# Performance work log

Measured on AMD Instinct MI355X. Metric: run time of the kernel, lower is better.

## Reference

```python
import jax, jax.numpy as jnp
import numpy as np

N_NODES = 100000


def _gcn_norm(edge_index, edge_weight, num_nodes):
    # PyG gcn_norm: add self-loops (weight 1), symmetric D^-1/2 (A+I) D^-1/2
    row, col = edge_index[0], edge_index[1]
    loop = jnp.arange(num_nodes, dtype=edge_index.dtype)
    row = jnp.concatenate([row, loop])
    col = jnp.concatenate([col, loop])
    w = jnp.concatenate([edge_weight, jnp.ones((num_nodes,), edge_weight.dtype)])
    deg = jax.ops.segment_sum(w, col, num_segments=num_nodes)
    dis = jnp.where(deg > 0, jax.lax.rsqrt(jnp.maximum(deg, 1e-12)), 0.0)
    norm = dis[row] * w * dis[col]
    return row, col, norm


def _gcn_conv(x, W, b, row, col, norm):
    h = x @ W                                   # transform first (small out dim)
    msg = norm[:, None] * h[row]                # gather + scale  [E+N, out]
    out = jax.ops.segment_sum(msg, col, num_segments=x.shape[0])  # scatter-add
    return out + b


def setup_inputs() -> dict:
    key = jax.random.key(0)
    k = jax.random.split(key, 6)
    N, E, F_IN, H, C = N_NODES, 3200000, 512, 16, 40
    x = jax.random.normal(k[0], (N, F_IN), dtype=jnp.float32)
    edge_index = jax.random.randint(k[1], (2, E), 0, N, dtype=jnp.int32)
    edge_weight = jax.random.uniform(k[2], (E,), dtype=jnp.float32)
    W1 = jax.random.normal(k[3], (F_IN, H), dtype=jnp.float32) * (1.0 / np.sqrt(F_IN))
    b1 = jnp.zeros((H,), jnp.float32)
    W2 = jax.random.normal(k[4], (H, C), dtype=jnp.float32) * (1.0 / np.sqrt(H))
    b2 = jnp.zeros((C,), jnp.float32)
    return {"x": x, "edge_index": edge_index, "edge_weight": edge_weight,
            "W1": W1, "b1": b1, "W2": W2, "b2": b2}


def reference(x, edge_index, edge_weight, W1, b1, W2, b2):
    row, col, norm = _gcn_norm(edge_index, edge_weight, N_NODES)
    h = jax.nn.relu(_gcn_conv(x, W1, b1, row, col, norm))
    # dropout is identity in eval mode
    h = _gcn_conv(h, W2, b2, row, col, norm)
    return jax.nn.log_softmax(h, axis=1)
```

## Files before the change

kernel.cpp:

```cpp
#include <hip/hip_runtime.h>
#include <math.h>

#define F_IN 512
#define HID  16
#define NCLS 40
#define NPB  128
#define NPW  2048
#define MAXBUK 1024
#define CAP  5120
#define SCAP 4608

typedef __attribute__((ext_vector_type(8))) short short8;
typedef __attribute__((ext_vector_type(4))) float floatx4;

__device__ __forceinline__ unsigned short bf16_rne(float f) {
    unsigned u = __float_as_uint(f);
    u += 0x7fffu + ((u >> 16) & 1u);
    return (unsigned short)(u >> 16);
}
__device__ __forceinline__ float bf16_f32(unsigned short s) {
    return __uint_as_float(((unsigned)s) << 16);
}

__global__ void k_zero(int* __restrict__ gcur, int nbuk) {
    int i = blockIdx.x * 256 + threadIdx.x;
    if (i < nbuk) gcur[i] = i * CAP;
}

__global__ void k_part(const int* __restrict__ row, const int* __restrict__ col,
                       const float* __restrict__ wt, int* __restrict__ gcur,
                       uint2* __restrict__ sedge, int E, int chunk, int nbuk) {
    __shared__ int lcnt[MAXBUK];
    __shared__ int lcur[MAXBUK];
    int t = threadIdx.x;
    int s = blockIdx.x * chunk;
    int e = s + chunk; if (e > E) e = E;
    if (e <= s) return;
    for (int i = t; i < nbuk; i += 256) lcnt[i] = 0;
    __syncthreads();
    for (int j = s + t; j < e; j += 256)
        atomicAdd(&lcnt[col[j] >> 7], 1);
    __syncthreads();
    for (int b = t; b < nbuk; b += 256) {
        int c = lcnt[b];
        lcur[b] = c ? atomicAdd(&gcur[b], c) : 0;
    }
    __syncthreads();
    for (int j = s + t; j < e; j += 256) {
        int r = row[j], cc = col[j];
        int b = cc >> 7;
        int slot = atomicAdd(&lcur[b], 1);
        if (slot < (b + 1) * CAP)
            sedge[slot] = make_uint2((unsigned)r | ((unsigned)(cc & (NPB - 1)) << 17),
                                     __float_as_uint(wt[j]));
    }
}

__global__ void k_sort(const uint2* __restrict__ sedge, const int* __restrict__ gcur,
                       uint2* __restrict__ sedge2, int2* __restrict__ rowse,
                       float* __restrict__ dis, int N, int nbuk) {
    __shared__ uint2 ebuf[SCAP];
    __shared__ int   cnt[NPB];
    __shared__ float wdeg[NPB];
    __shared__ int   scn[NPB];
    __shared__ int   cur[NPB];
    int b = blockIdx.x, t = threadIdx.x;
    if (t < NPB) { cnt[t] = 0; wdeg[t] = 1.0f; }
    __syncthreads();
    int s = b * CAP;
    int e = gcur[b];
    int n = e - s;
    bool fit = (n <= SCAP);
    for (int j = s + t; j < e; j += 256) {
        uint2 rec = sedge[j];
        if (fit) ebuf[j - s] = rec;
        int lc = rec.x >> 17;
        atomicAdd(&cnt[lc], 1);
        atomicAdd(&wdeg[lc], __uint_as_float(rec.y));
    }
    __syncthreads();
    if (t < NPB) scn[t] = cnt[t];
    __syncthreads();
    for (int off = 1; off < NPB; off <<= 1) {
        int a = (t < NPB && t >= off) ? scn[t - off] : 0;
        __syncthreads();
        if (t < NPB) scn[t] += a;
        __syncthreads();
    }
    if (t < NPB) {
        int excl = scn[t] - cnt[t];
        cur[t] = s + excl;
        int nn = b * NPB + t;
        if (nn < N) {
            rowse[nn] = make_int2(s + excl, s + excl + cnt[t]);
            dis[nn] = rsqrtf(wdeg[t]);
        }
    }
    __syncthreads();
    for (int i = t; i < n; i += 256) {
        uint2 rec = fit ? ebuf[i] : sedge[s + i];
        int lc = rec.x >> 17;
        int pos = atomicAdd(&cur[lc], 1);
        sedge2[pos] = make_uint2(rec.x & 0x1FFFF, rec.y);
    }
}

__global__ void k_xw1_mfma(const float* __restrict__ x, const float* __restrict__ W1,
                           const float* __restrict__ dis, float* __restrict__ h1,
                           int N, int nTiles) {
    __shared__ unsigned short wh[HID][F_IN + 8];
    __shared__ unsigned short wl[HID][F_IN + 8];
    for (int f = threadIdx.x; f < F_IN * HID; f += 256) {
        int k = f >> 4, h = f & 15;
        float v = W1[f];
        unsigned short hhi = bf16_rne(v);
        float rem = v - bf16_f32(hhi);
        wh[h][k] = hhi;
        wl[h][k] = (unsigned short)(__float_as_uint(rem) >> 16);
    }
    __syncthreads();

    int wave = threadIdx.x >> 6;
    int lane = threadIdx.x & 63;
    int tile = blockIdx.x * 4 + wave;
    if (tile >= nTiles) return;

    int m    = lane & 15;
    int quad = lane >> 4;
    int node = tile * 16 + m;
    if (node >= N) node = N - 1;
    const float* xr = x + (size_t)node * F_IN;

    floatx4 acc = {0.f, 0.f, 0.f, 0.f};

    #pragma unroll 4
    for (int s = 0; s < F_IN / 32; ++s) {
        int k0 = s * 32 + quad * 8;
        float4 v0 = *(const float4*)(xr + k0);
        float4 v1 = *(const float4*)(xr + k0 + 4);
        float xv[8] = {v0.x, v0.y, v0.z, v0.w, v1.x, v1.y, v1.z, v1.w};
        short8 ah, al;
        #pragma unroll
        for (int j = 0; j < 8; ++j) {
            unsigned u = __float_as_uint(xv[j]);
            ah[j] = (short)(u >> 16);
            float rem = xv[j] - __uint_as_float(u & 0xffff0000u);
            al[j] = (short)(__float_as_uint(rem) >> 16);
        }
        short8 bh = *(const short8*)&wh[m][k0];
        short8 bl = *(const short8*)&wl[m][k0];
        acc = __builtin_amdgcn_mfma_f32_16x16x32_bf16(ah, bh, acc, 0, 0, 0);
        acc = __builtin_amdgcn_mfma_f32_16x16x32_bf16(ah, bl, acc, 0, 0, 0);
        acc = __builtin_amdgcn_mfma_f32_16x16x32_bf16(al, bh, acc, 0, 0, 0);
    }

    int h = lane & 15;
    #pragma unroll
    for (int r = 0; r < 4; ++r) {
        int nrow = tile * 16 + quad * 4 + r;
        if (nrow < N) h1[(size_t)nrow * HID + h] = dis[nrow] * acc[r];
    }
}

__global__ void k_agg2(const uint2* __restrict__ sedge2, const int2* __restrict__ rowse,
                       const float* __restrict__ dis, const float* __restrict__ src,
                       const float* __restrict__ bias, float* __restrict__ dst,
                       int N, int relu, int postscale) {
    int g = (blockIdx.x * 256 + threadIdx.x) >> 4;
    int h = threadIdx.x & 15;
    if (g >= N) return;
    int2 se = rowse[g];
    int e1 = se.y;
    float acc = 0.f;
    int j = se.x;
    for (; j + 4 <= e1; j += 4) {
        uint2 r0 = sedge2[j + 0];
        uint2 r1 = sedge2[j + 1];
        uint2 r2 = sedge2[j + 2];
        uint2 r3 = sedge2[j + 3];
        float v0 = src[(size_t)r0.x * HID + h];
        float v1 = src[(size_t)r1.x * HID + h];
        float v2 = src[(size_t)r2.x * HID + h];
        float v3 = src[(size_t)r3.x * HID + h];
        acc = fmaf(__uint_as_float(r0.y), v0, acc);
        acc = fmaf(__uint_as_float(r1.y), v1, acc);
        acc = fmaf(__uint_as_float(r2.y), v2, acc);
        acc = fmaf(__uint_as_float(r3.y), v3, acc);
    }
    for (; j < e1; ++j) {
        uint2 r = sedge2[j];
        acc = fmaf(__uint_as_float(r.y), src[(size_t)r.x * HID + h], acc);
    }
    float d = dis[g];
    float v = d * (acc + src[(size_t)g * HID + h]);
    if (bias) v += bias[h];
    if (relu) v = v > 0.f ? v : 0.f;
    if (postscale) v *= d;
    dst[(size_t)g * HID + h] = v;
}

__global__ void k_final(const float* __restrict__ B, const float* __restrict__ W2,
                        const float* __restrict__ b2, float* __restrict__ out, int N) {
    __shared__ float w2s[HID * NCLS];
    __shared__ float b2s[NCLS];
    for (int f = threadIdx.x; f < HID * NCLS; f += 256) w2s[f] = W2[f];
    if (threadIdx.x < NCLS) b2s[threadIdx.x] = b2[threadIdx.x];
    __syncthreads();
    int nd = blockIdx.x * 256 + threadIdx.x;
    if (nd < N) {
        float a[HID];
        const float4* ap = (const float4*)(B + (size_t)nd * HID);
        #pragma unroll
        for (int q = 0; q < 4; ++q) {
            float4 v = ap[q];
            a[q * 4 + 0] = v.x; a[q * 4 + 1] = v.y;
            a[q * 4 + 2] = v.z; a[q * 4 + 3] = v.w;
        }
        float y[NCLS];
        #pragma unroll
        for (int c = 0; c < NCLS; ++c) y[c] = b2s[c];
        #pragma unroll
        for (int hh = 0; hh < HID; ++hh) {
            float av = a[hh];
            #pragma unroll
            for (int c = 0; c < NCLS; ++c) y[c] = fmaf(av, w2s[hh * NCLS + c], y[c]);
        }
        float m = y[0];
        #pragma unroll
        for (int c = 1; c < NCLS; ++c) m = fmaxf(m, y[c]);
        float sum = 0.f;
        #pragma unroll
        for (int c = 0; c < NCLS; ++c) sum += expf(y[c] - m);
        float bse = m + logf(sum);
        float* op = out + (size_t)nd * NCLS;
        #pragma unroll
        for (int c = 0; c < NCLS; ++c) op[c] = y[c] - bse;
    }
}

extern "C" void kernel_launch(void* const* d_in, const int* in_sizes, int n_in,
                              void* d_out, int out_size, void* d_ws, size_t ws_size,
                              hipStream_t stream) {
    const float* x  = (const float*)d_in[0];
    const int*   ei = (const int*)d_in[1];
    const float* ew = (const float*)d_in[2];
    const float* W1 = (const float*)d_in[3];
    const float* b1 = (const float*)d_in[4];
    const float* W2 = (const float*)d_in[5];
    const float* b2 = (const float*)d_in[6];
    float* out = (float*)d_out;

    int N = in_sizes[0] / F_IN;
    int E = in_sizes[2];
    const int* row = ei;
    const int* col = ei + E;

    int nbuk  = (N + NPB - 1) / NPB;
    int chunk = (E + NPW - 1) / NPW;

    char* w = (char*)d_ws;
    uint2* sedge  = (uint2*)w;                     size_t off = (size_t)nbuk * CAP * 8;
    uint2* sedge2 = (uint2*)(w + off);             off += (size_t)nbuk * CAP * 8;
    float* A      = (float*)(w + off);             off += (size_t)N * HID * 4;
    float* Bb     = (float*)(w + off);             off += (size_t)N * HID * 4;
    float* dis    = (float*)(w + off);             off += (size_t)N * 4;
    int2*  rowse  = (int2*)(w + off);              off += (size_t)N * 8;
    int*   gcur   = (int*)(w + off);               off += (size_t)nbuk * 4;

    dim3 blk(256);

    k_zero<<<dim3((nbuk + 255) / 256), blk, 0, stream>>>(gcur, nbuk);
    k_part<<<dim3(NPW), blk, 0, stream>>>(row, col, ew, gcur, sedge, E, chunk, nbuk);

    k_sort<<<dim3(nbuk), blk, 0, stream>>>(sedge, gcur, sedge2, rowse, dis, N, nbuk);

    int nTiles = (N + 15) / 16;
    int gT = (nTiles + 3) / 4;
    k_xw1_mfma<<<dim3(gT), blk, 0, stream>>>(x, W1, dis, A, N, nTiles);

    int gA = (N * HID + 255) / 256;
    k_agg2<<<dim3(gA), blk, 0, stream>>>(sedge2, rowse, dis, A, b1, Bb, N, 1, 1);
    k_agg2<<<dim3(gA), blk, 0, stream>>>(sedge2, rowse, dis, Bb, (const float*)nullptr, A, N, 0, 0);

    k_final<<<dim3((N + 255) / 256), blk, 0, stream>>>(A, W2, b2, out, N);
}
```

Measured before the change: 580.5 us.

## Replace single-pass bucket partition with two-level slice/bucket radix split

Result: faster. 527.7 us (-9.1%).

```diff
diff --git a/kernel.cpp b/kernel.cpp
--- a/kernel.cpp
+++ b/kernel.cpp
@@ -5,10 +5,13 @@
 #define HID  16
 #define NCLS 40
 #define NPB  128
+#define NSL  8
+#define BPS  98
+#define SLCAP 405504
+#define CAP  4608
 #define NPW  2048
-#define MAXBUK 1024
-#define CAP  5120
-#define SCAP 4608
+#define CPW2 256
+#define CH1  1600
 
 typedef __attribute__((ext_vector_type(8))) short short8;
 typedef __attribute__((ext_vector_type(4))) float floatx4;
@@ -22,58 +25,153 @@
     return __uint_as_float(((unsigned)s) << 16);
 }
 
-__global__ void k_zero(int* __restrict__ gcur, int nbuk) {
+__global__ void k_zero(int* __restrict__ gcur, int* __restrict__ scur, int nbuk) {
     int i = blockIdx.x * 256 + threadIdx.x;
     if (i < nbuk) gcur[i] = i * CAP;
-}
-
-__global__ void k_part(const int* __restrict__ row, const int* __restrict__ col,
-                       const float* __restrict__ wt, int* __restrict__ gcur,
-                       uint2* __restrict__ sedge, int E, int chunk, int nbuk) {
-    __shared__ int lcnt[MAXBUK];
-    __shared__ int lcur[MAXBUK];
+    if (i < NSL) scur[i] = i * SLCAP;
+}
+
+__global__ void k_split(const int* __restrict__ row, const int* __restrict__ col,
+                        const float* __restrict__ wt, int* __restrict__ scur,
+                        uint2* __restrict__ gstr, int E, int chunk) {
+    __shared__ uint2 recs[CH1];
+    __shared__ unsigned char bks[CH1];
+    __shared__ int cnt8[NSL], cur8[NSL], delta8[NSL];
     int t = threadIdx.x;
-    int s = blockIdx.x * chunk;
-    int e = s + chunk; if (e > E) e = E;
-    if (e <= s) return;
-    for (int i = t; i < nbuk; i += 256) lcnt[i] = 0;
-    __syncthreads();
-    for (int j = s + t; j < e; j += 256)
-        atomicAdd(&lcnt[col[j] >> 7], 1);
-    __syncthreads();
-    for (int b = t; b < nbuk; b += 256) {
-        int c = lcnt[b];
-        lcur[b] = c ? atomicAdd(&gcur[b], c) : 0;
-    }
-    __syncthreads();
-    for (int j = s + t; j < e; j += 256) {
-        int r = row[j], cc = col[j];
-        int b = cc >> 7;
-        int slot = atomicAdd(&lcur[b], 1);
-        if (slot < (b + 1) * CAP)
-            sedge[slot] = make_uint2((unsigned)r | ((unsigned)(cc & (NPB - 1)) << 17),
-                                     __float_as_uint(wt[j]));
+    int s0 = blockIdx.x * chunk;
+    int e0 = s0 + chunk; if (e0 > E) e0 = E;
+    int n = e0 - s0;
+    if (n <= 0) return;
+
+    if (n <= CH1) {
+        if (t < NSL) cnt8[t] = 0;
+        __syncthreads();
+        for (int j = s0 + t; j < e0; j += 256)
+            atomicAdd(&cnt8[(col[j] >> 7) / BPS], 1);
+        __syncthreads();
+        if (t == 0) {
+            int run = 0;
+            for (int i = 0; i < NSL; ++i) { cur8[i] = run; run += cnt8[i]; }
+        }
+        __syncthreads();
+        if (t < NSL) {
+            int c = cnt8[t];
+            int start = cur8[t];
+            int res = c ? atomicAdd(&scur[t], c) : 0;
+            delta8[t] = res - start;
+        }
+        __syncthreads();
+        for (int j = s0 + t; j < e0; j += 256) {
+            int r = row[j], cc = col[j];
+            int b = cc >> 7;
+            int sl = b / BPS;
+            int bsl = b - sl * BPS;
+            int slot = atomicAdd(&cur8[sl], 1);
+            recs[slot] = make_uint2((unsigned)r | ((unsigned)(cc & (NPB - 1)) << 17) |
+                                    ((unsigned)bsl << 24),
+                                    __float_as_uint(wt[j]));
+            bks[slot] = (unsigned char)sl;
+        }
+        __syncthreads();
+        for (int i = t; i < n; i += 256) {
+            int sl = bks[i];
+            int dst = delta8[sl] + i;
+            if ((unsigned)(dst - sl * SLCAP) < SLCAP) gstr[dst] = recs[i];
+        }
+    } else {
+        for (int j = s0 + t; j < e0; j += 256) {
+            int r = row[j], cc = col[j];
+            int b = cc >> 7;
+            int sl = b / BPS;
+            int bsl = b - sl * BPS;
+            int pos = atomicAdd(&scur[sl], 1);
+            if ((unsigned)(pos - sl * SLCAP) < SLCAP)
+                gstr[pos] = make_uint2((unsigned)r | ((unsigned)(cc & (NPB - 1)) << 17) |
+                                       ((unsigned)bsl << 24),
+                                       __float_as_uint(wt[j]));
+        }
+    }
+}
+
+__global__ void k_part2(const uint2* __restrict__ gstr, const int* __restrict__ scur,
+                        int* __restrict__ gcur, uint2* __restrict__ sedge, int nbuk) {
+    __shared__ uint2 recs[CH1];
+    __shared__ unsigned char bks[CH1];
+    __shared__ int lcnt[BPS], lcur[BPS], ldelta[BPS];
+    __shared__ int scn[128];
+    int t = threadIdx.x;
+    int sl = blockIdx.x & 7;
+    int ci = blockIdx.x >> 3;
+    int sbeg = sl * SLCAP;
+    int send = scur[sl];
+    int ns = send - sbeg;
+    int ch = (ns + CPW2 - 1) / CPW2;
+    int s0 = sbeg + ci * ch;
+    int e0 = s0 + ch; if (e0 > send) e0 = send;
+    int n = e0 - s0;
+    if (n <= 0) return;
+    for (int i = t; i < BPS; i += 256) lcnt[i] = 0;
+    __syncthreads();
+    for (int j = s0 + t; j < e0; j += 256)
+        atomicAdd(&lcnt[gstr[j].x >> 24], 1);
+    __syncthreads();
+    if (t < 128) scn[t] = (t < BPS) ? lcnt[t] : 0;
+    __syncthreads();
+    for (int off = 1; off < 128; off <<= 1) {
+        int a = (t < 128 && t >= off) ? scn[t - off] : 0;
+        __syncthreads();
+        if (t < 128) scn[t] += a;
+        __syncthreads();
+    }
+    if (t < BPS) {
+        int c = lcnt[t];
+        int start = scn[t] - c;
+        lcur[t] = start;
+        int res = c ? atomicAdd(&gcur[sl * BPS + t], c) : 0;
+        ldelta[t] = res - start;
+    }
+    __syncthreads();
+    for (int j = s0 + t; j < e0; j += 256) {
+        uint2 rec = gstr[j];
+        int bsl = rec.x >> 24;
+        int slot = atomicAdd(&lcur[bsl], 1);
+        recs[slot] = rec;
+        bks[slot] = (unsigned char)bsl;
+    }
+    __syncthreads();
+    for (int i = t; i < n; i += 256) {
+        int bsl = bks[i];
+        int gb = sl * BPS + bsl;
+        int dst = ldelta[bsl] + i;
+        if (dst < (gb + 1) * CAP) {
+            uint2 rr = recs[i];
+            rr.x &= 0x00FFFFFFu;
+            sedge[dst] = rr;
+        }
     }
 }
 
 __global__ void k_sort(const uint2* __restrict__ sedge, const int* __restrict__ gcur,
                        uint2* __restrict__ sedge2, int2* __restrict__ rowse,
                        float* __restrict__ dis, int N, int nbuk) {
-    __shared__ uint2 ebuf[SCAP];
+    __shared__ uint2 ebuf[CAP];
     __shared__ int   cnt[NPB];
     __shared__ float wdeg[NPB];
     __shared__ int   scn[NPB];
     __shared__ int   cur[NPB];
-    int b = blockIdx.x, t = threadIdx.x;
+    int sl = blockIdx.x & 7;
+    int bi = blockIdx.x >> 3;
+    int b = sl * BPS + bi;
+    if (bi >= BPS || b >= nbuk) return;
+    int t = threadIdx.x;
     if (t < NPB) { cnt[t] = 0; wdeg[t] = 1.0f; }
     __syncthreads();
     int s = b * CAP;
     int e = gcur[b];
     int n = e - s;
-    bool fit = (n <= SCAP);
     for (int j = s + t; j < e; j += 256) {
         uint2 rec = sedge[j];
-        if (fit) ebuf[j - s] = rec;
+        ebuf[j - s] = rec;
         int lc = rec.x >> 17;
         atomicAdd(&cnt[lc], 1);
         atomicAdd(&wdeg[lc], __uint_as_float(rec.y));
@@ -98,7 +196,7 @@
     }
     __syncthreads();
     for (int i = t; i < n; i += 256) {
-        uint2 rec = fit ? ebuf[i] : sedge[s + i];
+        uint2 rec = ebuf[i];
         int lc = rec.x >> 17;
         int pos = atomicAdd(&cur[lc], 1);
         sedge2[pos] = make_uint2(rec.x & 0x1FFFF, rec.y);
@@ -165,10 +263,14 @@
 __global__ void k_agg2(const uint2* __restrict__ sedge2, const int2* __restrict__ rowse,
                        const float* __restrict__ dis, const float* __restrict__ src,
                        const float* __restrict__ bias, float* __restrict__ dst,
-                       int N, int relu, int postscale) {
-    int g = (blockIdx.x * 256 + threadIdx.x) >> 4;
+                       int N, int nbuk, int relu, int postscale) {
+    int sl  = blockIdx.x & 7;
+    int loc = blockIdx.x >> 3;
+    int b   = sl * BPS + (loc >> 3);
+    int sub = loc & 7;
+    int g = b * NPB + sub * 16 + (threadIdx.x >> 4);
     int h = threadIdx.x & 15;
-    if (g >= N) return;
+    if (b >= nbuk || g >= N) return;
     int2 se = rowse[g];
     int e1 = se.y;
     float acc = 0.f;
@@ -259,28 +361,30 @@
     int chunk = (E + NPW - 1) / NPW;
 
     char* w = (char*)d_ws;
-    uint2* sedge  = (uint2*)w;                     size_t off = (size_t)nbuk * CAP * 8;
+    uint2* gstr   = (uint2*)w;                     size_t off = (size_t)NSL * SLCAP * 8;
+    uint2* sedge  = (uint2*)(w + off);             off += (size_t)nbuk * CAP * 8;
     uint2* sedge2 = (uint2*)(w + off);             off += (size_t)nbuk * CAP * 8;
     float* A      = (float*)(w + off);             off += (size_t)N * HID * 4;
     float* Bb     = (float*)(w + off);             off += (size_t)N * HID * 4;
     float* dis    = (float*)(w + off);             off += (size_t)N * 4;
     int2*  rowse  = (int2*)(w + off);              off += (size_t)N * 8;
     int*   gcur   = (int*)(w + off);               off += (size_t)nbuk * 4;
+    int*   scur   = (int*)(w + off);               off += (size_t)NSL * 4;
 
     dim3 blk(256);
 
-    k_zero<<<dim3((nbuk + 255) / 256), blk, 0, stream>>>(gcur, nbuk);
-    k_part<<<dim3(NPW), blk, 0, stream>>>(row, col, ew, gcur, sedge, E, chunk, nbuk);
-
-    k_sort<<<dim3(nbuk), blk, 0, stream>>>(sedge, gcur, sedge2, rowse, dis, N, nbuk);
+    k_zero<<<dim3((nbuk + 255) / 256), blk, 0, stream>>>(gcur, scur, nbuk);
+    k_split<<<dim3(NPW), blk, 0, stream>>>(row, col, ew, scur, gstr, E, chunk);
+    k_part2<<<dim3(NSL * CPW2), blk, 0, stream>>>(gstr, scur, gcur, sedge, nbuk);
+
+    k_sort<<<dim3(NSL * BPS), blk, 0, stream>>>(sedge, gcur, sedge2, rowse, dis, N, nbuk);
 
     int nTiles = (N + 15) / 16;
     int gT = (nTiles + 3) / 4;
     k_xw1_mfma<<<dim3(gT), blk, 0, stream>>>(x, W1, dis, A, N, nTiles);
 
-    int gA = (N * HID + 255) / 256;
-    k_agg2<<<dim3(gA), blk, 0, stream>>>(sedge2, rowse, dis, A, b1, Bb, N, 1, 1);
-    k_agg2<<<dim3(gA), blk, 0, stream>>>(sedge2, rowse, dis, Bb, (const float*)nullptr, A, N, 0, 0);
+    k_agg2<<<dim3(NSL * BPS * 8), blk, 0, stream>>>(sedge2, rowse, dis, A, b1, Bb, N, nbuk, 1, 1);
+    k_agg2<<<dim3(NSL * BPS * 8), blk, 0, stream>>>(sedge2, rowse, dis, Bb, (const float*)nullptr, A, N, nbuk, 0, 0);
 
     k_final<<<dim3((N + 255) / 256), blk, 0, stream>>>(A, W2, b2, out, N);
 }
```
